# Kernel tuning notes

Measured on AMD Instinct MI355X. Metric: run time of the kernel, lower is better.

## Reference

```python
import jax, jax.numpy as jnp
import numpy as np

E, B, D, T = 8, 4096, 2048, 2048
H = D // 2 + T // 2  # expert hidden dim = 2048
TOP_K = 2


def setup_inputs() -> dict:
    key = jax.random.key(0)
    ks = jax.random.split(key, 5)
    s_in = 1.0 / np.sqrt(D)
    s_h = 1.0 / np.sqrt(H)
    return {
        "xs": jax.random.normal(ks[0], (E, B, D), dtype=jnp.float32),
        "Wg": jax.random.normal(ks[1], (D,), dtype=jnp.float32) * s_in,
        "bg": jnp.zeros((1,), dtype=jnp.float32),
        "W1": jax.random.normal(ks[2], (E, D, H), dtype=jnp.float32) * s_in,
        "b1": jnp.zeros((E, H), dtype=jnp.float32),
        "W2": jax.random.normal(ks[3], (E, H, T), dtype=jnp.float32) * s_h,
        "b2": jnp.zeros((E, T), dtype=jnp.float32),
    }


def reference(xs, Wg, bg, W1, b1, W2, b2):
    # Gating: logits[b, e] = x[e][b] @ Wg + bg  -> [B, E]
    logits = jnp.einsum("ebd,d->be", xs, Wg) + bg
    probs = jax.nn.softmax(logits, axis=1)
    top_k_values, top_k_indices = jax.lax.top_k(probs, TOP_K)  # [B, K]

    # Dense expert compute over each expert's own input stream.
    # hidden[e, b, h] = relu(x[e] @ W1[e] + b1[e]); out[e, b, t] = hidden @ W2[e] + b2[e]
    hidden = jax.nn.relu(jnp.einsum("ebd,edh->ebh", xs, W1) + b1[:, None, :])
    expert_out = jnp.einsum("ebh,eht->ebt", hidden, W2) + b2[:, None, :]  # [E, B, T]

    # Gather the top-k experts per token. In the original, masked-dense compute
    # + output mask is mathematically identical to this gather.
    per_token = jnp.transpose(expert_out, (1, 0, 2))  # [B, E, T]
    selected = jnp.take_along_axis(per_token, top_k_indices[:, :, None], axis=1)  # [B, K, T]

    out = jnp.sum(top_k_values[:, :, None] * selected, axis=1)  # [B, T]
    return out, top_k_values
```

## Files before the change

kernel.cpp:

```cpp
#include <hip/hip_runtime.h>
#include <hip/hip_bf16.h>
#include <stdint.h>

#define E_ 8
#define B_ 4096
#define D_ 2048
#define T_ 2048
#define H_ 2048
#define KDIM 2048
#define NDIM 2048
#define NROWS (E_ * 1024 + 128)

typedef __attribute__((ext_vector_type(4))) float f32x4;
typedef __attribute__((ext_vector_type(4))) unsigned short u16x4;
typedef __attribute__((ext_vector_type(8))) unsigned short u16x8;
typedef __attribute__((ext_vector_type(8))) __bf16 bf16x8;

__device__ __forceinline__ unsigned short f2bf(float f) {
    __hip_bfloat16 h = __float2bfloat16(f);
    return __builtin_bit_cast(unsigned short, h);
}

__device__ __forceinline__ void gload_lds16(const void* g, void* lds) {
    __builtin_amdgcn_global_load_lds(
        (const __attribute__((address_space(1))) void*)g,
        (__attribute__((address_space(3))) void*)lds, 16, 0, 0);
}

__global__ __launch_bounds__(256) void moe_gating(
    const float* __restrict__ xs, const float* __restrict__ Wg,
    const float* __restrict__ bg, float* __restrict__ out_topk,
    float* __restrict__ prob_slot, int* __restrict__ counts,
    int* __restrict__ slot_of)
{
    const int b = blockIdx.x;
    const int t = threadIdx.x;
    const int wave = t >> 6, lane = t & 63;
    __shared__ float red[E_][4];

    const f32x4 wg0 = ((const f32x4*)Wg)[t];
    const f32x4 wg1 = ((const f32x4*)Wg)[t + 256];

    for (int e = 0; e < E_; ++e) {
        const f32x4* xr = (const f32x4*)(xs + ((size_t)e * B_ + b) * D_);
        f32x4 a0 = __builtin_nontemporal_load(&xr[t]);
        f32x4 a1 = __builtin_nontemporal_load(&xr[t + 256]);
        float p = a0.x*wg0.x + a0.y*wg0.y + a0.z*wg0.z + a0.w*wg0.w
                + a1.x*wg1.x + a1.y*wg1.y + a1.z*wg1.z + a1.w*wg1.w;
        #pragma unroll
        for (int off = 32; off >= 1; off >>= 1) p += __shfl_xor(p, off);
        if (lane == 0) red[e][wave] = p;
    }
    __syncthreads();
    if (t == 0) {
        float pr[E_];
        float mx = -3.0e38f;
        #pragma unroll
        for (int e = 0; e < E_; ++e) {
            pr[e] = red[e][0] + red[e][1] + red[e][2] + red[e][3] + bg[0];
            mx = fmaxf(mx, pr[e]);
        }
        float s = 0.f;
        #pragma unroll
        for (int e = 0; e < E_; ++e) { pr[e] = expf(pr[e] - mx); s += pr[e]; }
        float inv = 1.0f / s;
        #pragma unroll
        for (int e = 0; e < E_; ++e) pr[e] *= inv;
        int i0 = 0;
        #pragma unroll
        for (int e = 1; e < E_; ++e) if (pr[e] > pr[i0]) i0 = e;
        int i1 = (i0 == 0) ? 1 : 0;
        #pragma unroll
        for (int e = 0; e < E_; ++e) { if (e != i0 && pr[e] > pr[i1]) i1 = e; }
        float p0 = pr[i0], p1 = pr[i1];
        out_topk[2*b]    = p0;
        out_topk[2*b+1]  = p1;
        prob_slot[2*b]   = p0;
        prob_slot[2*b+1] = p1;
        int pos0 = atomicAdd(&counts[i0], 1);
        slot_of[i0 * B_ + pos0] = 2*b;
        int pos1 = atomicAdd(&counts[i1], 1);
        slot_of[i1 * B_ + pos1] = 2*b + 1;
    }
}

__global__ void build_tiles(const int* __restrict__ counts,
                            int* __restrict__ tiles, int* __restrict__ ebase)
{
    if (threadIdx.x == 0 && blockIdx.x == 0) {
        int n = 0, base = 0;
        for (int e = 0; e < E_; ++e) {
            ebase[e] = base;
            int te = (counts[e] + 127) >> 7;
            for (int m = 0; m < te; ++m) tiles[1 + n++] = (e << 16) | m;
            base += counts[e];
        }
        tiles[0] = n;
    }
}

__global__ __launch_bounds__(256) void pack_A(
    const float* __restrict__ xs, const int* __restrict__ slot_of,
    const int* __restrict__ counts, const int* __restrict__ ebase,
    const float* __restrict__ prob_slot, unsigned short* __restrict__ Ax,
    int* __restrict__ tokid, float* __restrict__ prob_pk)
{
    const int e = blockIdx.x >> 12;
    const int i = blockIdx.x & 4095;
    if (i >= counts[e]) return;
    const int slot = slot_of[e * B_ + i];
    const int b = slot >> 1;
    const int g = ebase[e] + i;
    const int t = threadIdx.x;

    const f32x4* src = (const f32x4*)(xs + ((size_t)e * B_ + b) * D_);
    f32x4 v0 = src[2*t], v1 = src[2*t + 1];
    u16x8 w;
    w[0]=f2bf(v0.x); w[1]=f2bf(v0.y); w[2]=f2bf(v0.z); w[3]=f2bf(v0.w);
    w[4]=f2bf(v1.x); w[5]=f2bf(v1.y); w[6]=f2bf(v1.z); w[7]=f2bf(v1.w);
    ((u16x8*)(Ax + (size_t)g * D_))[t] = w;
    if (t == 0) { tokid[g] = b; prob_pk[g] = prob_slot[slot]; }
}

template<int DUAL>
__global__ __launch_bounds__(256) void wtrans(
    const float* __restrict__ Wa, const float* __restrict__ Wb,
    unsigned short* __restrict__ Wta, unsigned short* __restrict__ Wtb)
{
    const int z  = blockIdx.z;
    const int e  = DUAL ? (z & 7) : z;
    const float* W = (DUAL && (z >> 3)) ? Wb : Wa;
    unsigned short* Wt = (DUAL && (z >> 3)) ? Wtb : Wta;
    const int kb = blockIdx.x * 64;
    const int nb = blockIdx.y * 64;
    const int t  = threadIdx.x;
    __shared__ float tile[64][68];

    const float* src = W + ((size_t)e * KDIM + kb) * NDIM + nb;
    {
        const int kr = t >> 2, nc = (t & 3) * 16;
        #pragma unroll
        for (int j = 0; j < 4; ++j) {
            f32x4 v = __builtin_nontemporal_load(
                (const f32x4*)(src + (size_t)kr * NDIM + nc + j * 4));
            *(f32x4*)&tile[kr][nc + j * 4] = v;
        }
    }
    __syncthreads();
    {
        const int nn = t >> 2, kc = (t & 3) * 16;
        unsigned short wbuf[16];
        #pragma unroll
        for (int j = 0; j < 16; ++j) wbuf[j] = f2bf(tile[kc + j][nn]);
        unsigned short* dst = Wt + ((size_t)e * NDIM + nb + nn) * KDIM + kb + kc;
        *(u16x8*)dst       = *(const u16x8*)&wbuf[0];
        *((u16x8*)dst + 1) = *(const u16x8*)&wbuf[8];
    }
}

#define BAR  __builtin_amdgcn_s_barrier()

template<int LAYER>
__global__ __launch_bounds__(256, 2) void moe_gemm(
    const unsigned short* __restrict__ Abuf,
    const unsigned short* __restrict__ Wt,
    const float* __restrict__ bias,
    const int* __restrict__ counts,
    const int* __restrict__ tiles,
    const int* __restrict__ ebase,
    const int* __restrict__ tokid,
    const float* __restrict__ prob_pk,
    unsigned short* __restrict__ hidden_out,
    float* __restrict__ out)
{
    const int nMt = tiles[0];
    const int bid = blockIdx.x;
    const int mt  = bid >> 4;
    const int np  = bid & 15;
    if (mt >= nMt) return;
    const int info = tiles[1 + mt];
    const int e    = info >> 16;
    const int mloc = (info & 0xffff) * 128;
    const int gm0  = ebase[e] + mloc;
    const int n0   = np * 128;
    const int n_e  = counts[e];

    const int t = threadIdx.x;
    const int lane = t & 63;
    const int w = t >> 6;
    const int wm = (w >> 1) * 64;
    const int wn = (w & 1) * 64;
    const int lg = lane >> 4;

    __shared__ u16x8 As[2048];
    __shared__ u16x8 Bs[2048];

    const int kSrc = (((t & 7) ^ ((t >> 3) & 7)) << 3);
    const unsigned short* aSrc[4];
    const unsigned short* bSrc[4];
    #pragma unroll
    for (int i = 0; i < 4; ++i) {
        const int r = i * 32 + (t >> 3);
        aSrc[i] = Abuf + (size_t)(gm0 + r) * KDIM + kSrc;
        bSrc[i] = Wt + ((size_t)e * NDIM + n0 + r) * KDIM + kSrc;
    }
    u16x8* aDst = &As[0];
    u16x8* bDst = &Bs[0];

    f32x4 acc[4][4];
    #pragma unroll
    for (int i = 0; i < 4; ++i)
        #pragma unroll
        for (int j = 0; j < 4; ++j) {
            f32x4 z = {0.f, 0.f, 0.f, 0.f};
            acc[i][j] = z;
        }

#define STG(BUF, KT) do{ \
    _Pragma("unroll") \
    for (int i = 0; i < 4; ++i) { \
        gload_lds16(aSrc[i] + (KT)*64, aDst + (BUF)*1024 + t + i*256); \
        gload_lds16(bSrc[i] + (KT)*64, bDst + (BUF)*1024 + t + i*256); } }while(0)

    STG(0, 0);
    asm volatile("s_waitcnt vmcnt(0)" ::: "memory");
    BAR;

    int cur = 0;
    for (int kt = 0; kt < 32; ++kt) {
        int tn = kt + 1; if (tn > 31) tn = 31;
        STG(cur ^ 1, tn);

        #pragma unroll
        for (int kk = 0; kk < 2; ++kk) {
            const int kb = kk * 4 + lg;
            bf16x8 af[4], bq[4];
            #pragma unroll
            for (int mi = 0; mi < 4; ++mi) {
                const int row = wm + mi * 16 + (lane & 15);
                af[mi] = __builtin_bit_cast(bf16x8,
                    As[cur * 1024 + row * 8 + (kb ^ (row & 7))]);
            }
            #pragma unroll
            for (int ni = 0; ni < 4; ++ni) {
                const int row = wn + ni * 16 + (lane & 15);
                bq[ni] = __builtin_bit_cast(bf16x8,
                    Bs[cur * 1024 + row * 8 + (kb ^ (row & 7))]);
            }
            #pragma unroll
            for (int mi = 0; mi < 4; ++mi)
                #pragma unroll
                for (int ni = 0; ni < 4; ++ni)
                    acc[mi][ni] = __builtin_amdgcn_mfma_f32_16x16x32_bf16(
                        af[mi], bq[ni], acc[mi][ni], 0, 0, 0);
        }

        asm volatile("s_waitcnt vmcnt(0)" ::: "memory");
        BAR;
        cur ^= 1;
    }

    #pragma unroll
    for (int mi = 0; mi < 4; ++mi) {
        #pragma unroll
        for (int rr = 0; rr < 4; ++rr) {
            const int rloc = wm + mi * 16 + ((lane >> 4) << 2) + rr;
            if (mloc + rloc >= n_e) continue;
            const int g = gm0 + rloc;
            #pragma unroll
            for (int ni = 0; ni < 4; ++ni) {
                const int col = n0 + wn + ni * 16 + (lane & 15);
                float v = acc[mi][ni][rr];
                if (LAYER == 1) {
                    v += bias[e * NDIM + col];
                    v = fmaxf(v, 0.f);
                    hidden_out[(size_t)g * H_ + col] = f2bf(v);
                } else {
                    v = (v + bias[e * NDIM + col]) * prob_pk[g];
                    atomicAdd(&out[(size_t)tokid[g] * T_ + col], v);
                }
            }
        }
    }
#undef STG
}

extern "C" void kernel_launch(void* const* d_in, const int* in_sizes, int n_in,
                              void* d_out, int out_size, void* d_ws, size_t ws_size,
                              hipStream_t stream)
{
    const float* xs = (const float*)d_in[0];
    const float* Wg = (const float*)d_in[1];
    const float* bg = (const float*)d_in[2];
    const float* W1 = (const float*)d_in[3];
    const float* b1 = (const float*)d_in[4];
    const float* W2 = (const float*)d_in[5];
    const float* b2 = (const float*)d_in[6];

    float* out      = (float*)d_out;
    float* out_topk = out + (size_t)B_ * T_;

    char* ws = (char*)d_ws;
    int*   counts    = (int*)ws;
    int*   tiles     = (int*)(ws + 256);
    int*   ebase     = (int*)(ws + 768);
    int*   slot_of   = (int*)(ws + 1024);
    float* prob_slot = (float*)(ws + 1024 + E_ * B_ * 4);
    size_t off = 1024 + (size_t)E_ * B_ * 4 + 2 * B_ * 4;
    off = (off + 255) & ~(size_t)255;
    int*   tokid   = (int*)(ws + off);   off += (size_t)NROWS * 4;
    float* prob_pk = (float*)(ws + off); off += (size_t)NROWS * 4;
    off = (off + 255) & ~(size_t)255;
    unsigned short* Ax     = (unsigned short*)(ws + off); off += (size_t)NROWS * D_ * 2;
    unsigned short* hidden = (unsigned short*)(ws + off); off += (size_t)NROWS * H_ * 2;
    unsigned short* Wt1    = (unsigned short*)(ws + off); off += (size_t)E_ * KDIM * NDIM * 2;
    size_t off_big = off + (size_t)E_ * KDIM * NDIM * 2;
    unsigned short* Wt2 = (unsigned short*)(ws + off);

    const bool big = (ws_size >= off_big);

    hipMemsetAsync(counts, 0, 256, stream);
    hipMemsetAsync(out, 0, (size_t)B_ * T_ * sizeof(float), stream);

    dim3 blk(256);
    dim3 ggrid(72 * 16);
    dim3 pgrid(E_ * 4096);

    if (big) {
        dim3 tgrid(32, 32, 16);
        wtrans<1><<<tgrid, blk, 0, stream>>>(W1, W2, Wt1, Wt2);
        moe_gating<<<dim3(B_), blk, 0, stream>>>(
            xs, Wg, bg, out_topk, prob_slot, counts, slot_of);
        build_tiles<<<dim3(1), dim3(64), 0, stream>>>(counts, tiles, ebase);
        pack_A<<<pgrid, blk, 0, stream>>>(
            xs, slot_of, counts, ebase, prob_slot, Ax, tokid, prob_pk);
        moe_gemm<1><<<ggrid, blk, 0, stream>>>(
            Ax, Wt1, b1, counts, tiles, ebase, tokid, prob_pk, hidden, nullptr);
        moe_gemm<2><<<ggrid, blk, 0, stream>>>(
            hidden, Wt2, b2, counts, tiles, ebase, tokid, prob_pk, nullptr, out);
    } else {
        dim3 tgrid(32, 32, E_);
        moe_gating<<<dim3(B_), blk, 0, stream>>>(
            xs, Wg, bg, out_topk, prob_slot, counts, slot_of);
        build_tiles<<<dim3(1), dim3(64), 0, stream>>>(counts, tiles, ebase);
        pack_A<<<pgrid, blk, 0, stream>>>(
            xs, slot_of, counts, ebase, prob_slot, Ax, tokid, prob_pk);
        wtrans<0><<<tgrid, blk, 0, stream>>>(W1, nullptr, Wt1, nullptr);
        moe_gemm<1><<<ggrid, blk, 0, stream>>>(
            Ax, Wt1, b1, counts, tiles, ebase, tokid, prob_pk, hidden, nullptr);
        wtrans<0><<<tgrid, blk, 0, stream>>>(W2, nullptr, Wt1, nullptr);
        moe_gemm<2><<<ggrid, blk, 0, stream>>>(
            hidden, Wt1, b2, counts, tiles, ebase, tokid, prob_pk, nullptr, out);
    }
}
```

Baseline: 547.8 us.

## Enlarge MoE GEMM tiles to 256x256 with 4-stage pipeline, fuse bf16 pack into gating

```diff
diff --git a/kernel.cpp b/kernel.cpp
--- a/kernel.cpp
+++ b/kernel.cpp
@@ -9,10 +9,9 @@
 #define H_ 2048
 #define KDIM 2048
 #define NDIM 2048
-#define NROWS (E_ * 1024 + 128)
+#define NROWS (E_ * 1024 + 256)
 
 typedef __attribute__((ext_vector_type(4))) float f32x4;
-typedef __attribute__((ext_vector_type(4))) unsigned short u16x4;
 typedef __attribute__((ext_vector_type(8))) unsigned short u16x8;
 typedef __attribute__((ext_vector_type(8))) __bf16 bf16x8;
 
@@ -31,22 +30,25 @@
     const float* __restrict__ xs, const float* __restrict__ Wg,
     const float* __restrict__ bg, float* __restrict__ out_topk,
     float* __restrict__ prob_slot, int* __restrict__ counts,
-    int* __restrict__ slot_of)
+    int* __restrict__ slot_of, unsigned short* __restrict__ A1)
 {
     const int b = blockIdx.x;
     const int t = threadIdx.x;
     const int wave = t >> 6, lane = t & 63;
     __shared__ float red[E_][4];
+    __shared__ int sh_i0, sh_i1;
 
     const f32x4 wg0 = ((const f32x4*)Wg)[t];
     const f32x4 wg1 = ((const f32x4*)Wg)[t + 256];
 
+    f32x4 xa[E_], xb[E_];
+    #pragma unroll
     for (int e = 0; e < E_; ++e) {
         const f32x4* xr = (const f32x4*)(xs + ((size_t)e * B_ + b) * D_);
-        f32x4 a0 = __builtin_nontemporal_load(&xr[t]);
-        f32x4 a1 = __builtin_nontemporal_load(&xr[t + 256]);
-        float p = a0.x*wg0.x + a0.y*wg0.y + a0.z*wg0.z + a0.w*wg0.w
-                + a1.x*wg1.x + a1.y*wg1.y + a1.z*wg1.z + a1.w*wg1.w;
+        xa[e] = __builtin_nontemporal_load(&xr[t]);
+        xb[e] = __builtin_nontemporal_load(&xr[t + 256]);
+        float p = xa[e].x*wg0.x + xa[e].y*wg0.y + xa[e].z*wg0.z + xa[e].w*wg0.w
+                + xb[e].x*wg1.x + xb[e].y*wg1.y + xb[e].z*wg1.z + xb[e].w*wg1.w;
         #pragma unroll
         for (int off = 32; off >= 1; off >>= 1) p += __shfl_xor(p, off);
         if (lane == 0) red[e][wave] = p;
@@ -81,7 +83,27 @@
         slot_of[i0 * B_ + pos0] = 2*b;
         int pos1 = atomicAdd(&counts[i1], 1);
         slot_of[i1 * B_ + pos1] = 2*b + 1;
-    }
+        sh_i0 = i0; sh_i1 = i1;
+    }
+    __syncthreads();
+    const int i0 = sh_i0, i1 = sh_i1;
+    f32x4 s0a = xa[0], s0b = xb[0], s1a = xa[0], s1b = xb[0];
+    #pragma unroll
+    for (int e = 0; e < E_; ++e) {
+        if (i0 == e) { s0a = xa[e]; s0b = xb[e]; }
+        if (i1 == e) { s1a = xa[e]; s1b = xb[e]; }
+    }
+    u16x8 w;
+    w[0]=f2bf(s0a.x); w[1]=f2bf(s0a.y); w[2]=f2bf(s0a.z); w[3]=f2bf(s0a.w);
+    w[4]=f2bf(s0b.x); w[5]=f2bf(s0b.y); w[6]=f2bf(s0b.z); w[7]=f2bf(s0b.w);
+    {
+    }
+    unsigned short* r0 = A1 + (size_t)(2*b) * D_;
+    unsigned short* r1 = A1 + (size_t)(2*b+1) * D_;
+    r0[4*t+0]=f2bf(s0a.x); r0[4*t+1]=f2bf(s0a.y); r0[4*t+2]=f2bf(s0a.z); r0[4*t+3]=f2bf(s0a.w);
+    r0[1024+4*t+0]=f2bf(s0b.x); r0[1024+4*t+1]=f2bf(s0b.y); r0[1024+4*t+2]=f2bf(s0b.z); r0[1024+4*t+3]=f2bf(s0b.w);
+    r1[4*t+0]=f2bf(s1a.x); r1[4*t+1]=f2bf(s1a.y); r1[4*t+2]=f2bf(s1a.z); r1[4*t+3]=f2bf(s1a.w);
+    r1[1024+4*t+0]=f2bf(s1b.x); r1[1024+4*t+1]=f2bf(s1b.y); r1[1024+4*t+2]=f2bf(s1b.z); r1[1024+4*t+3]=f2bf(s1b.w);
 }
 
 __global__ void build_tiles(const int* __restrict__ counts,
@@ -91,7 +113,7 @@
         int n = 0, base = 0;
         for (int e = 0; e < E_; ++e) {
             ebase[e] = base;
-            int te = (counts[e] + 127) >> 7;
+            int te = (counts[e] + 255) >> 8;
             for (int m = 0; m < te; ++m) tiles[1 + n++] = (e << 16) | m;
             base += counts[e];
         }
@@ -100,7 +122,7 @@
 }
 
 __global__ __launch_bounds__(256) void pack_A(
-    const float* __restrict__ xs, const int* __restrict__ slot_of,
+    const unsigned short* __restrict__ A1, const int* __restrict__ slot_of,
     const int* __restrict__ counts, const int* __restrict__ ebase,
     const float* __restrict__ prob_slot, unsigned short* __restrict__ Ax,
     int* __restrict__ tokid, float* __restrict__ prob_pk)
@@ -109,17 +131,11 @@
     const int i = blockIdx.x & 4095;
     if (i >= counts[e]) return;
     const int slot = slot_of[e * B_ + i];
-    const int b = slot >> 1;
     const int g = ebase[e] + i;
     const int t = threadIdx.x;
-
-    const f32x4* src = (const f32x4*)(xs + ((size_t)e * B_ + b) * D_);
-    f32x4 v0 = src[2*t], v1 = src[2*t + 1];
-    u16x8 w;
-    w[0]=f2bf(v0.x); w[1]=f2bf(v0.y); w[2]=f2bf(v0.z); w[3]=f2bf(v0.w);
-    w[4]=f2bf(v1.x); w[5]=f2bf(v1.y); w[6]=f2bf(v1.z); w[7]=f2bf(v1.w);
-    ((u16x8*)(Ax + (size_t)g * D_))[t] = w;
-    if (t == 0) { tokid[g] = b; prob_pk[g] = prob_slot[slot]; }
+    ((u16x8*)(Ax + (size_t)g * D_))[t] =
+        ((const u16x8*)(A1 + (size_t)slot * D_))[t];
+    if (t == 0) { tokid[g] = slot >> 1; prob_pk[g] = prob_slot[slot]; }
 }
 
 template<int DUAL>
@@ -161,7 +177,7 @@
 #define BAR  __builtin_amdgcn_s_barrier()
 
 template<int LAYER>
-__global__ __launch_bounds__(256, 2) void moe_gemm(
+__global__ __launch_bounds__(1024, 4) void moe_gemm(
     const unsigned short* __restrict__ Abuf,
     const unsigned short* __restrict__ Wt,
     const float* __restrict__ bias,
@@ -175,37 +191,34 @@
 {
     const int nMt = tiles[0];
     const int bid = blockIdx.x;
-    const int mt  = bid >> 4;
-    const int np  = bid & 15;
+    const int mt  = bid >> 3;
+    const int np  = bid & 7;
     if (mt >= nMt) return;
     const int info = tiles[1 + mt];
     const int e    = info >> 16;
-    const int mloc = (info & 0xffff) * 128;
+    const int mloc = (info & 0xffff) * 256;
     const int gm0  = ebase[e] + mloc;
-    const int n0   = np * 128;
+    const int n0   = np * 256;
     const int n_e  = counts[e];
 
     const int t = threadIdx.x;
     const int lane = t & 63;
     const int w = t >> 6;
-    const int wm = (w >> 1) * 64;
-    const int wn = (w & 1) * 64;
+    const int wm = (w >> 2) * 64;
+    const int wn = (w & 3) * 64;
     const int lg = lane >> 4;
 
-    __shared__ u16x8 As[2048];
-    __shared__ u16x8 Bs[2048];
-
-    const int kSrc = (((t & 7) ^ ((t >> 3) & 7)) << 3);
-    const unsigned short* aSrc[4];
-    const unsigned short* bSrc[4];
-    #pragma unroll
-    for (int i = 0; i < 4; ++i) {
-        const int r = i * 32 + (t >> 3);
-        aSrc[i] = Abuf + (size_t)(gm0 + r) * KDIM + kSrc;
-        bSrc[i] = Wt + ((size_t)e * NDIM + n0 + r) * KDIM + kSrc;
-    }
-    u16x8* aDst = &As[0];
-    u16x8* bDst = &Bs[0];
+    __shared__ u16x8 As[4 * 1024];
+    __shared__ u16x8 Bs[4 * 1024];
+
+    const int ksw = (((t & 3) ^ ((t >> 3) & 3)) << 3);
+    const unsigned short* aptr = Abuf + (size_t)(gm0 + (t >> 2)) * KDIM + ksw;
+    const unsigned short* bptr =
+        Wt + ((size_t)e * NDIM + n0 + (t >> 2)) * KDIM + ksw;
+
+#define STG(BUF, KT) do{ \
+    gload_lds16(aptr + (KT)*32, &As[(BUF)*1024 + w*64]); \
+    gload_lds16(bptr + (KT)*32, &Bs[(BUF)*1024 + w*64]); }while(0)
 
     f32x4 acc[4][4];
     #pragma unroll
@@ -216,49 +229,33 @@
             acc[i][j] = z;
         }
 
-#define STG(BUF, KT) do{ \
-    _Pragma("unroll") \
-    for (int i = 0; i < 4; ++i) { \
-        gload_lds16(aSrc[i] + (KT)*64, aDst + (BUF)*1024 + t + i*256); \
-        gload_lds16(bSrc[i] + (KT)*64, bDst + (BUF)*1024 + t + i*256); } }while(0)
-
-    STG(0, 0);
-    asm volatile("s_waitcnt vmcnt(0)" ::: "memory");
-    BAR;
-
-    int cur = 0;
-    for (int kt = 0; kt < 32; ++kt) {
-        int tn = kt + 1; if (tn > 31) tn = 31;
-        STG(cur ^ 1, tn);
-
-        #pragma unroll
-        for (int kk = 0; kk < 2; ++kk) {
-            const int kb = kk * 4 + lg;
-            bf16x8 af[4], bq[4];
-            #pragma unroll
-            for (int mi = 0; mi < 4; ++mi) {
-                const int row = wm + mi * 16 + (lane & 15);
-                af[mi] = __builtin_bit_cast(bf16x8,
-                    As[cur * 1024 + row * 8 + (kb ^ (row & 7))]);
-            }
-            #pragma unroll
-            for (int ni = 0; ni < 4; ++ni) {
-                const int row = wn + ni * 16 + (lane & 15);
-                bq[ni] = __builtin_bit_cast(bf16x8,
-                    Bs[cur * 1024 + row * 8 + (kb ^ (row & 7))]);
-            }
+    STG(0, 0); STG(1, 1); STG(2, 2);
+
+    const int usw = (lane >> 1) & 3;
+    for (int kt = 0; kt < 64; ++kt) {
+        asm volatile("s_waitcnt vmcnt(4)" ::: "memory");
+        BAR;
+        int tn = kt + 3; if (tn > 63) tn = 63;
+        STG((kt + 3) & 3, tn);
+
+        const int base = (kt & 3) * 1024;
+        bf16x8 af[4];
+        #pragma unroll
+        for (int mi = 0; mi < 4; ++mi) {
+            const int row = wm + mi * 16 + (lane & 15);
+            af[mi] = __builtin_bit_cast(bf16x8, As[base + row * 4 + (lg ^ usw)]);
+        }
+        #pragma unroll
+        for (int ni = 0; ni < 4; ++ni) {
+            const int row = wn + ni * 16 + (lane & 15);
+            bf16x8 bq = __builtin_bit_cast(bf16x8, Bs[base + row * 4 + (lg ^ usw)]);
             #pragma unroll
             for (int mi = 0; mi < 4; ++mi)
-                #pragma unroll
-                for (int ni = 0; ni < 4; ++ni)
-                    acc[mi][ni] = __builtin_amdgcn_mfma_f32_16x16x32_bf16(
-                        af[mi], bq[ni], acc[mi][ni], 0, 0, 0);
-        }
-
-        asm volatile("s_waitcnt vmcnt(0)" ::: "memory");
-        BAR;
-        cur ^= 1;
-    }
+                acc[mi][ni] = __builtin_amdgcn_mfma_f32_16x16x32_bf16(
+                    af[mi], bq, acc[mi][ni], 0, 0, 0);
+        }
+    }
+    asm volatile("s_waitcnt vmcnt(0)" ::: "memory");
 
     #pragma unroll
     for (int mi = 0; mi < 4; ++mi) {
@@ -311,6 +308,7 @@
     int*   tokid   = (int*)(ws + off);   off += (size_t)NROWS * 4;
     float* prob_pk = (float*)(ws + off); off += (size_t)NROWS * 4;
     off = (off + 255) & ~(size_t)255;
+    unsigned short* A1     = (unsigned short*)(ws + off); off += (size_t)2 * B_ * D_ * 2;
     unsigned short* Ax     = (unsigned short*)(ws + off); off += (size_t)NROWS * D_ * 2;
     unsigned short* hidden = (unsigned short*)(ws + off); off += (size_t)NROWS * H_ * 2;
     unsigned short* Wt1    = (unsigned short*)(ws + off); off += (size_t)E_ * KDIM * NDIM * 2;
@@ -322,34 +320,34 @@
     hipMemsetAsync(counts, 0, 256, stream);
     hipMemsetAsync(out, 0, (size_t)B_ * T_ * sizeof(float), stream);
 
-    dim3 blk(256);
-    dim3 ggrid(72 * 16);
+    dim3 blk(256), gblk(1024);
+    dim3 ggrid(39 * 8);
     dim3 pgrid(E_ * 4096);
 
     if (big) {
         dim3 tgrid(32, 32, 16);
         wtrans<1><<<tgrid, blk, 0, stream>>>(W1, W2, Wt1, Wt2);
         moe_gating<<<dim3(B_), blk, 0, stream>>>(
-            xs, Wg, bg, out_topk, prob_slot, counts, slot_of);
+            xs, Wg, bg, out_topk, prob_slot, counts, slot_of, A1);
         build_tiles<<<dim3(1), dim3(64), 0, stream>>>(counts, tiles, ebase);
         pack_A<<<pgrid, blk, 0, stream>>>(
-            xs, slot_of, counts, ebase, prob_slot, Ax, tokid, prob_pk);
-        moe_gemm<1><<<ggrid, blk, 0, stream>>>(
+            A1, slot_of, counts, ebase, prob_slot, Ax, tokid, prob_pk);
+        moe_gemm<1><<<ggrid, gblk, 0, stream>>>(
             Ax, Wt1, b1, counts, tiles, ebase, tokid, prob_pk, hidden, nullptr);
-        moe_gemm<2><<<ggrid, blk, 0, stream>>>(
+        moe_gemm<2><<<ggrid, gblk, 0, stream>>>(
             hidden, Wt2, b2, counts, tiles, ebase, tokid, prob_pk, nullptr, out);
     } else {
         dim3 tgrid(32, 32, E_);
         moe_gating<<<dim3(B_), blk, 0, stream>>>(
-            xs, Wg, bg, out_topk, prob_slot, counts, slot_of);
+            xs, Wg, bg, out_topk, prob_slot, counts, slot_of, A1);
         build_tiles<<<dim3(1), dim3(64), 0, stream>>>(counts, tiles, ebase);
         pack_A<<<pgrid, blk, 0, stream>>>(
-            xs, slot_of, counts, ebase, prob_slot, Ax, tokid, prob_pk);
+            A1, slot_of, counts, ebase, prob_slot, Ax, tokid, prob_pk);
         wtrans<0><<<tgrid, blk, 0, stream>>>(W1, nullptr, Wt1, nullptr);
-        moe_gemm<1><<<ggrid, blk, 0, stream>>>(
+        moe_gemm<1><<<ggrid, gblk, 0, stream>>>(
             Ax, Wt1, b1, counts, tiles, ebase, tokid, prob_pk, hidden, nullptr);
         wtrans<0><<<tgrid, blk, 0, stream>>>(W2, nullptr, Wt1, nullptr);
-        moe_gemm<2><<<ggrid, blk, 0, stream>>>(
+        moe_gemm<2><<<ggrid, gblk, 0, stream>>>(
             hidden, Wt1, b2, counts, tiles, ebase, tokid, prob_pk, nullptr, out);
     }
 }
```

Result: no change. 540.8 us (-1.3%).
